# Performance work log

Hardware: AMD Instinct MI355X
Metric: run time of the kernel (lower is better)

Reference implementation:

```python
import jax, jax.numpy as jnp
import numpy as np

N = 100000      # nodes
E = 1600000     # edges (avg degree 16)
IN = 128        # in_channels
H = 128         # hidden
C = 40          # num_classes
NCOMM = 1000    # number of communities


def setup_inputs() -> dict:
    key = jax.random.key(0)
    ks = jax.random.split(key, 6)
    x = jax.random.normal(ks[0], (N, IN), dtype=jnp.float32)
    edge_index = jax.random.randint(ks[1], (2, E), 0, N, dtype=jnp.int64)
    community = jax.random.randint(ks[2], (N,), 0, NCOMM, dtype=jnp.int64)
    W_in = jax.random.normal(ks[3], (2 * IN, H), dtype=jnp.float32) * 0.05
    b_in = jnp.zeros((H,), dtype=jnp.float32)
    W1 = jax.random.normal(ks[4], (H, H), dtype=jnp.float32) * 0.05
    b1 = jnp.zeros((H,), dtype=jnp.float32)
    W2 = jax.random.normal(ks[5], (H, C), dtype=jnp.float32) * 0.05
    b2 = jnp.zeros((C,), dtype=jnp.float32)
    return {"x": x, "edge_index": edge_index, "community": community,
            "W_in": W_in, "b_in": b_in, "W1": W1, "b1": b1, "W2": W2, "b2": b2}


def _gcn_conv(h, W, b, src, dst, n):
    """PyG GCNConv: transform, add self-loops, symmetric deg^-1/2 normalization."""
    hw = h @ W  # [n, out]
    deg = jax.ops.segment_sum(jnp.ones((src.shape[0],), hw.dtype), dst, num_segments=n) + 1.0  # +1 self-loop
    dis = jax.lax.rsqrt(deg)                      # deg >= 1 always
    norm = dis[src] * dis[dst]                    # [E]
    agg = jax.ops.segment_sum(hw[src] * norm[:, None], dst, num_segments=n)
    # self-loop contribution: norm_ii = dis[i]^2 = 1/deg[i]
    return agg + hw * (1.0 / deg)[:, None] + b


def reference(x, edge_index, community, W_in, b_in, W1, b1, W2, b2):
    n = x.shape[0]
    # CommunityPassing(aggr='mean'): per-community mean, broadcast back to nodes
    csum = jax.ops.segment_sum(x, community, num_segments=NCOMM)
    ccnt = jax.ops.segment_sum(jnp.ones((n,), x.dtype), community, num_segments=NCOMM)
    cmean = csum / jnp.maximum(ccnt, 1.0)[:, None]
    x_comm = cmean[community]                     # [n, IN]
    h = jnp.concatenate([x, x_comm], axis=-1)     # [n, 2*IN]
    h = jax.nn.relu(h @ W_in + b_in)              # dropout is identity at eval
    src, dst = edge_index[0], edge_index[1]
    h = jax.nn.relu(_gcn_conv(h, W1, b1, src, dst, n))
    out = _gcn_conv(h, W2, b2, src, dst, n)
    return out
```

## Files before the change

kernel.cpp:

```cpp
#include <hip/hip_runtime.h>
#include <cstdint>
#include <cstddef>

#define NNODES 100000
#define NEDGES 1600000
#define INCH   128
#define HID    128
#define NCLS   40
#define NCOMM_ 1000

#define NBLK  128
#define EPB   (NEDGES/NBLK)
#define NBUCK ((NNODES+255)/256)
#define NCNT  (NBLK*NBUCK)

typedef unsigned int uint32;
typedef unsigned short ushort16;
typedef short s16x8 __attribute__((ext_vector_type(8)));
typedef float f32x4 __attribute__((ext_vector_type(4)));

static __device__ __forceinline__ float4 ld4(const float* p){ return *reinterpret_cast<const float4*>(p); }

static __device__ __forceinline__ unsigned short f2b(float f){
  union{float f; uint32 u;} v; v.f=f;
  uint32 r = v.u + 0x7fffu + ((v.u>>16)&1u);
  return (unsigned short)(r>>16);
}
static __device__ __forceinline__ float b2f(unsigned short h){
  union{uint32 u; float f;} v; v.u = ((uint32)h)<<16; return v.f;
}
static __device__ __forceinline__ float lo16f(uint32 u){ return __int_as_float((int)(u<<16)); }
static __device__ __forceinline__ float hi16f(uint32 u){ return __int_as_float((int)(u&0xffff0000u)); }

static __device__ __forceinline__ void acc8(float* a, uint4 v, float nr){
  a[0]=fmaf(lo16f(v.x),nr,a[0]); a[1]=fmaf(hi16f(v.x),nr,a[1]);
  a[2]=fmaf(lo16f(v.y),nr,a[2]); a[3]=fmaf(hi16f(v.y),nr,a[3]);
  a[4]=fmaf(lo16f(v.z),nr,a[4]); a[5]=fmaf(hi16f(v.z),nr,a[5]);
  a[6]=fmaf(lo16f(v.w),nr,a[6]); a[7]=fmaf(hi16f(v.w),nr,a[7]);
}
static __device__ __forceinline__ void acc4(float* a, uint2 v, float nr){
  a[0]=fmaf(lo16f(v.x),nr,a[0]); a[1]=fmaf(hi16f(v.x),nr,a[1]);
  a[2]=fmaf(lo16f(v.y),nr,a[2]); a[3]=fmaf(hi16f(v.y),nr,a[3]);
}

__global__ void k_ccomm(const int* __restrict__ comm, int* __restrict__ ccnt){
  int i=blockIdx.x*blockDim.x+threadIdx.x;
  if(i<NNODES) atomicAdd(&ccnt[comm[i]],1);
}

__global__ __launch_bounds__(256) void k_bcnt(const int* __restrict__ ei, int* __restrict__ cnt){
  __shared__ int h[NBUCK];
  int t=threadIdx.x, blk=blockIdx.x;
  for(int i=t;i<NBUCK;i+=256) h[i]=0;
  __syncthreads();
  int base=blk*EPB;
  for(int j=t;j<EPB;j+=256){
    int d=ei[NEDGES+base+j];
    atomicAdd(&h[d>>8],1);
  }
  __syncthreads();
  for(int i=t;i<NBUCK;i+=256) cnt[i*NBLK+blk]=h[i];
}

__global__ void k_scan1(const int* __restrict__ in, int n, int* __restrict__ part){
  int t=threadIdx.x, b=blockIdx.x;
  int base=b*1024+t*4, s=0;
  #pragma unroll
  for(int j=0;j<4;j++){ int i=base+j; if(i<n) s+=in[i]; }
  #pragma unroll
  for(int off=32;off>0;off>>=1) s+=__shfl_down(s,off,64);
  __shared__ int wm[4];
  if((t&63)==0) wm[t>>6]=s;
  __syncthreads();
  if(t==0) part[b]=wm[0]+wm[1]+wm[2]+wm[3];
}

__global__ void k_scan2(int* __restrict__ part, int P){
  __shared__ int sm[256];
  int t=threadIdx.x;
  int v=(t<P)?part[t]:0;
  sm[t]=v; __syncthreads();
  #pragma unroll
  for(int off=1;off<256;off<<=1){
    int u=(t>=off)?sm[t-off]:0;
    __syncthreads();
    sm[t]+=u;
    __syncthreads();
  }
  if(t<P) part[t]=(t==0)?0:sm[t-1];
  if(t==0) part[P]=sm[255];
}

__global__ void k_scan3(const int* __restrict__ in, int n, const int* __restrict__ part, int P,
                        int* __restrict__ out){
  int t=threadIdx.x,b=blockIdx.x;
  int base=b*1024+t*4;
  int v[4], ts=0;
  #pragma unroll
  for(int j=0;j<4;j++){ v[j]=(base+j<n)?in[base+j]:0; ts+=v[j]; }
  int lane=t&63, w=t>>6, sc=ts;
  #pragma unroll
  for(int off=1;off<64;off<<=1){ int u=__shfl_up(sc,off,64); if(lane>=off) sc+=u; }
  __shared__ int wm[4];
  if(lane==63) wm[w]=sc;
  __syncthreads();
  int woff=0;
  for(int i=0;i<w;i++) woff+=wm[i];
  int pos=part[b]+woff+sc-ts;
  #pragma unroll
  for(int j=0;j<4;j++){ if(base+j<n) out[base+j]=pos; pos+=v[j]; }
  if(b==0 && t==0) out[n]=part[P];
}

__global__ void k_bextract(const int* __restrict__ cntx, int* __restrict__ brow, int* __restrict__ rp){
  int b=blockIdx.x*blockDim.x+threadIdx.x;
  if(b<NBUCK) brow[b]=cntx[b*NBLK];
  if(b==NBUCK){ brow[NBUCK]=NEDGES; rp[NNODES]=NEDGES; }
}

__global__ __launch_bounds__(256) void k_bscatter(const int* __restrict__ ei, const int* __restrict__ cntx,
                                                  int2* __restrict__ ebuf){
  __shared__ int offs[NBUCK];
  int t=threadIdx.x, blk=blockIdx.x;
  for(int i=t;i<NBUCK;i+=256) offs[i]=cntx[i*NBLK+blk];
  __syncthreads();
  int base=blk*EPB;
  for(int j=t;j<EPB;j+=256){
    int e=base+j;
    int s=ei[e], d=ei[NEDGES+e];
    int p=atomicAdd(&offs[d>>8],1);
    ebuf[p]=make_int2(s,d);
  }
}

__global__ __launch_bounds__(256) void k_bcsr(const int2* __restrict__ ebuf, const int* __restrict__ brow,
                                              int* __restrict__ rp, float* __restrict__ dis,
                                              float* __restrict__ dinv, int* __restrict__ esrc){
  __shared__ int lcnt[256], lrp[256], lfill[256];
  int b=blockIdx.x, t=threadIdx.x;
  int e0=brow[b], e1=brow[b+1];
  int n0=b*256, nloc=min(256, NNODES-n0);
  lcnt[t]=0;
  __syncthreads();
  for(int e=e0+t;e<e1;e+=256){
    int d=ebuf[e].y;
    atomicAdd(&lcnt[d&255],1);
  }
  __syncthreads();
  lrp[t]=lcnt[t]; __syncthreads();
  #pragma unroll
  for(int off=1;off<256;off<<=1){
    int u=(t>=off)?lrp[t-off]:0;
    __syncthreads();
    lrp[t]+=u;
    __syncthreads();
  }
  int excl=lrp[t]-lcnt[t];
  __syncthreads();
  lrp[t]=e0+excl;
  lfill[t]=0;
  if(t<nloc){
    int gid=n0+t;
    rp[gid]=e0+excl;
    float dd=(float)(lcnt[t]+1);
    dis[gid]=rsqrtf(dd);
    dinv[gid]=1.0f/dd;
  }
  __syncthreads();
  for(int e=e0+t;e<e1;e+=256){
    int2 r=ebuf[e];
    int lr=r.y&255;
    int slot=atomicAdd(&lfill[lr],1);
    esrc[lrp[lr]+slot]=r.x;
  }
}

__global__ void k_fill_comm(const int* __restrict__ comm, const int* __restrict__ crow, int* __restrict__ cfill,
                            int* __restrict__ cnode){
  int i=blockIdx.x*blockDim.x+threadIdx.x;
  if(i<NNODES){
    int c=comm[i];
    int p=crow[c]+atomicAdd(&cfill[c],1);
    cnode[p]=i;
  }
}

__global__ void k_comm_mean(const float* __restrict__ x, const int* __restrict__ crow,
                            const int* __restrict__ cnode, float* __restrict__ cmean){
  int c=blockIdx.x; int f=threadIdx.x;
  int a=crow[c], b=crow[c+1];
  float s=0.f;
  for(int j=a;j<b;j++){
    int nd=cnode[j];
    s += x[(size_t)nd*INCH + f];
  }
  float cnt=(float)(b-a);
  cmean[(size_t)c*INCH + f] = s / fmaxf(cnt,1.0f);
}

__global__ void k_wprep(const float* __restrict__ W_in, const float* __restrict__ W1, const float* __restrict__ W2,
                        ushort16* __restrict__ Wt0h, ushort16* __restrict__ Wt0l,
                        ushort16* __restrict__ Wt1h, ushort16* __restrict__ Wt1l,
                        ushort16* __restrict__ Wt2h, ushort16* __restrict__ Wt2l){
  int t = blockIdx.x*256 + threadIdx.x;
  float v; ushort16* ph; ushort16* pl; int off;
  if(t < 32768){
    int n=t>>8, k=t&255; v=W_in[k*128+n]; ph=Wt0h; pl=Wt0l; off=t;
  } else if(t < 49152){
    int u=t-32768; int n=u>>7, k=u&127; v=W1[k*128+n]; ph=Wt1h; pl=Wt1l; off=u;
  } else if(t < 55296){
    int u=t-49152; int n=u>>7, k=u&127; v=(n<40)?W2[k*40+n]:0.f; ph=Wt2h; pl=Wt2l; off=u;
  } else return;
  unsigned short h=f2b(v); unsigned short lo=f2b(v-b2f(h));
  ph[off]=h; pl[off]=lo;
}

template<int K, bool CONCAT, bool BIAS, bool RELU>
__global__ __launch_bounds__(256) void k_mm128(const void* __restrict__ A0, const float* __restrict__ A1f,
                                               const int* __restrict__ comm,
                                               const ushort16* __restrict__ WtH, const ushort16* __restrict__ WtL,
                                               const float* __restrict__ bias,
                                               ushort16* __restrict__ out, int M){
  __shared__ __align__(16) ushort16 As[128*40];
  __shared__ __align__(16) ushort16 Bh[128*40];
  __shared__ __align__(16) ushort16 Bl[128*40];
  int t=threadIdx.x;
  int m0=blockIdx.x*128;
  int lane=t&63, w=t>>6;
  int g=lane>>4, r15=lane&15;

  f32x4 acc0[8], acc1[8];
  #pragma unroll
  for(int i=0;i<8;i++){ acc0[i]=(f32x4){0,0,0,0}; acc1[i]=(f32x4){0,0,0,0}; }

  int ar = t>>1, ko = (t&1)*16;

  for(int kc=0;kc<K;kc+=32){
    __syncthreads();
    {
      s16x8 q0, q1;
      int gr = m0 + ar;
      if(gr < M){
        if(CONCAT){
          const float* src = (kc<128) ? ((const float*)A0 + (size_t)gr*128 + kc + ko)
                                      : (A1f + (size_t)comm[gr]*128 + (kc-128) + ko);
          float4 p0=ld4(src), p1=ld4(src+4), p2=ld4(src+8), p3=ld4(src+12);
          q0[0]=(short)f2b(p0.x); q0[1]=(short)f2b(p0.y); q0[2]=(short)f2b(p0.z); q0[3]=(short)f2b(p0.w);
          q0[4]=(short)f2b(p1.x); q0[5]=(short)f2b(p1.y); q0[6]=(short)f2b(p1.z); q0[7]=(short)f2b(p1.w);
          q1[0]=(short)f2b(p2.x); q1[1]=(short)f2b(p2.y); q1[2]=(short)f2b(p2.z); q1[3]=(short)f2b(p2.w);
          q1[4]=(short)f2b(p3.x); q1[5]=(short)f2b(p3.y); q1[6]=(short)f2b(p3.z); q1[7]=(short)f2b(p3.w);
        } else {
          const ushort16* srcu = (const ushort16*)A0 + (size_t)gr*K + kc + ko;
          q0 = *(const s16x8*)srcu;
          q1 = *(const s16x8*)(srcu+8);
        }
      } else {
        q0=(s16x8){0,0,0,0,0,0,0,0}; q1=q0;
      }
      ushort16* dst=&As[ar*40+ko];
      *(s16x8*)dst=q0; *(s16x8*)(dst+8)=q1;
    }
    {
      const ushort16* sh=&WtH[(size_t)ar*K + kc + ko];
      s16x8 b0=*(const s16x8*)sh, b1=*(const s16x8*)(sh+8);
      ushort16* dh=&Bh[ar*40+ko];
      *(s16x8*)dh=b0; *(s16x8*)(dh+8)=b1;
      const ushort16* sl=&WtL[(size_t)ar*K + kc + ko];
      s16x8 c0=*(const s16x8*)sl, c1=*(const s16x8*)(sl+8);
      ushort16* dl=&Bl[ar*40+ko];
      *(s16x8*)dl=c0; *(s16x8*)(dl+8)=c1;
    }
    __syncthreads();
    s16x8 a0 = *(const s16x8*)&As[(w*32      + r15)*40 + g*8];
    s16x8 a1 = *(const s16x8*)&As[(w*32 + 16 + r15)*40 + g*8];
    #pragma unroll
    for(int tn=0;tn<8;tn++){
      s16x8 bh = *(const s16x8*)&Bh[(tn*16 + r15)*40 + g*8];
      s16x8 bl = *(const s16x8*)&Bl[(tn*16 + r15)*40 + g*8];
      acc0[tn] = __builtin_amdgcn_mfma_f32_16x16x32_bf16(a0, bh, acc0[tn], 0,0,0);
      acc0[tn] = __builtin_amdgcn_mfma_f32_16x16x32_bf16(a0, bl, acc0[tn], 0,0,0);
      acc1[tn] = __builtin_amdgcn_mfma_f32_16x16x32_bf16(a1, bh, acc1[tn], 0,0,0);
      acc1[tn] = __builtin_amdgcn_mfma_f32_16x16x32_bf16(a1, bl, acc1[tn], 0,0,0);
    }
  }

  #pragma unroll
  for(int tn=0;tn<8;tn++){
    int col = tn*16 + r15;
    float bv = BIAS ? bias[col] : 0.f;
    #pragma unroll
    for(int rr=0;rr<4;rr++){
      int row0 = m0 + w*32 + g*4 + rr;
      if(row0 < M){
        float v = acc0[tn][rr] + bv;
        if(RELU) v = fmaxf(v, 0.f);
        out[(size_t)row0*128 + col] = f2b(v);
      }
      int row1 = m0 + w*32 + 16 + g*4 + rr;
      if(row1 < M){
        float v = acc1[tn][rr] + bv;
        if(RELU) v = fmaxf(v, 0.f);
        out[(size_t)row1*128 + col] = f2b(v);
      }
    }
  }
}

__global__ __launch_bounds__(256) void k_mm40(const ushort16* __restrict__ A0,
                                              const ushort16* __restrict__ WtH, const ushort16* __restrict__ WtL,
                                              ushort16* __restrict__ out, int M){
  __shared__ __align__(16) ushort16 As[128*40];
  __shared__ __align__(16) ushort16 Bh[48*40];
  __shared__ __align__(16) ushort16 Bl[48*40];
  int t=threadIdx.x;
  int m0=blockIdx.x*128;
  int lane=t&63, w=t>>6;
  int g=lane>>4, r15=lane&15;

  f32x4 acc0[3], acc1[3];
  #pragma unroll
  for(int i=0;i<3;i++){ acc0[i]=(f32x4){0,0,0,0}; acc1[i]=(f32x4){0,0,0,0}; }

  int ar=t>>1, ko=(t&1)*16;

  for(int kc=0;kc<128;kc+=32){
    __syncthreads();
    {
      s16x8 q0,q1;
      int gr=m0+ar;
      if(gr<M){
        const ushort16* srcu = A0 + (size_t)gr*128 + kc + ko;
        q0=*(const s16x8*)srcu; q1=*(const s16x8*)(srcu+8);
      } else { q0=(s16x8){0,0,0,0,0,0,0,0}; q1=q0; }
      ushort16* dst=&As[ar*40+ko];
      *(s16x8*)dst=q0; *(s16x8*)(dst+8)=q1;
    }
    if(t<96){
      int n=t>>1, k2=(t&1)*16;
      const ushort16* sh=&WtH[(size_t)n*128 + kc + k2];
      s16x8 b0=*(const s16x8*)sh, b1=*(const s16x8*)(sh+8);
      ushort16* dh=&Bh[n*40+k2];
      *(s16x8*)dh=b0; *(s16x8*)(dh+8)=b1;
    } else if(t<192){
      int u=t-96; int n=u>>1, k2=(u&1)*16;
      const ushort16* sl=&WtL[(size_t)n*128 + kc + k2];
      s16x8 c0=*(const s16x8*)sl, c1=*(const s16x8*)(sl+8);
      ushort16* dl=&Bl[n*40+k2];
      *(s16x8*)dl=c0; *(s16x8*)(dl+8)=c1;
    }
    __syncthreads();
    s16x8 a0=*(const s16x8*)&As[(w*32      + r15)*40 + g*8];
    s16x8 a1=*(const s16x8*)&As[(w*32 + 16 + r15)*40 + g*8];
    #pragma unroll
    for(int tn=0;tn<3;tn++){
      s16x8 bh=*(const s16x8*)&Bh[(tn*16 + r15)*40 + g*8];
      s16x8 bl=*(const s16x8*)&Bl[(tn*16 + r15)*40 + g*8];
      acc0[tn]=__builtin_amdgcn_mfma_f32_16x16x32_bf16(a0,bh,acc0[tn],0,0,0);
      acc0[tn]=__builtin_amdgcn_mfma_f32_16x16x32_bf16(a0,bl,acc0[tn],0,0,0);
      acc1[tn]=__builtin_amdgcn_mfma_f32_16x16x32_bf16(a1,bh,acc1[tn],0,0,0);
      acc1[tn]=__builtin_amdgcn_mfma_f32_16x16x32_bf16(a1,bl,acc1[tn],0,0,0);
    }
  }
  #pragma unroll
  for(int tn=0;tn<3;tn++){
    int col=tn*16+r15;
    if(col<NCLS){
      #pragma unroll
      for(int rr=0;rr<4;rr++){
        int row0=m0+w*32+g*4+rr;
        if(row0<M) out[(size_t)row0*NCLS+col]=f2b(acc0[tn][rr]);
        int row1=m0+w*32+16+g*4+rr;
        if(row1<M) out[(size_t)row1*NCLS+col]=f2b(acc1[tn][rr]);
      }
    }
  }
}

__global__ __launch_bounds__(256) void k_agg_h(const uint4* __restrict__ hwv, const int* __restrict__ rp,
                                               const int* __restrict__ esrc,
                                               const float* __restrict__ dis, const float* __restrict__ dinv,
                                               const float* __restrict__ bias, uint4* __restrict__ h1v){
  int w=threadIdx.x>>6;
  int i=blockIdx.x*4+w;
  if(i>=NNODES) return;
  int lane=threadIdx.x&63;
  int g=lane>>4, f=lane&15;
  int e0=rp[i], e1=rp[i+1];
  float di=dis[i];
  float a[8]={0,0,0,0,0,0,0,0};
  int e=e0+g;
  for(; e+4<e1; e+=8){
    int s0=esrc[e], s1=esrc[e+4];
    float n0=di*dis[s0], n1=di*dis[s1];
    uint4 v0=hwv[(size_t)s0*16+f];
    uint4 v1=hwv[(size_t)s1*16+f];
    acc8(a,v0,n0); acc8(a,v1,n1);
  }
  if(e<e1){
    int s0=esrc[e];
    float n0=di*dis[s0];
    uint4 v0=hwv[(size_t)s0*16+f];
    acc8(a,v0,n0);
  }
  #pragma unroll
  for(int k=0;k<8;k++){
    a[k]+=__shfl_xor(a[k],16);
    a[k]+=__shfl_xor(a[k],32);
  }
  if(g==0){
    uint4 sv=hwv[(size_t)i*16+f];
    float dv=dinv[i];
    float4 bA=*reinterpret_cast<const float4*>(&bias[8*f]);
    float4 bB=*reinterpret_cast<const float4*>(&bias[8*f+4]);
    float o0=fmaxf(fmaf(lo16f(sv.x),dv,a[0])+bA.x,0.f);
    float o1=fmaxf(fmaf(hi16f(sv.x),dv,a[1])+bA.y,0.f);
    float o2=fmaxf(fmaf(lo16f(sv.y),dv,a[2])+bA.z,0.f);
    float o3=fmaxf(fmaf(hi16f(sv.y),dv,a[3])+bA.w,0.f);
    float o4=fmaxf(fmaf(lo16f(sv.z),dv,a[4])+bB.x,0.f);
    float o5=fmaxf(fmaf(hi16f(sv.z),dv,a[5])+bB.y,0.f);
    float o6=fmaxf(fmaf(lo16f(sv.w),dv,a[6])+bB.z,0.f);
    float o7=fmaxf(fmaf(hi16f(sv.w),dv,a[7])+bB.w,0.f);
    uint4 o;
    o.x=((uint32)f2b(o1)<<16)|(uint32)f2b(o0);
    o.y=((uint32)f2b(o3)<<16)|(uint32)f2b(o2);
    o.z=((uint32)f2b(o5)<<16)|(uint32)f2b(o4);
    o.w=((uint32)f2b(o7)<<16)|(uint32)f2b(o6);
    h1v[(size_t)i*16+f]=o;
  }
}

__global__ __launch_bounds__(256) void k_agg_out(const uint2* __restrict__ hv, const int* __restrict__ rp,
                                                 const int* __restrict__ esrc,
                                                 const float* __restrict__ dis, const float* __restrict__ dinv,
                                                 const float* __restrict__ bias, float* __restrict__ out){
  int w=threadIdx.x>>6;
  int i=blockIdx.x*4+w;
  if(i>=NNODES) return;
  int lane=threadIdx.x&63;
  int g=lane>>4, f=lane&15;
  bool act=(f<10);
  int e0=rp[i], e1=rp[i+1];
  float di=dis[i];
  float a[4]={0,0,0,0};
  int e=e0+g;
  for(; e+4<e1; e+=8){
    int s0=esrc[e], s1=esrc[e+4];
    float n0=di*dis[s0], n1=di*dis[s1];
    if(act){
      uint2 v0=hv[(size_t)s0*10+f];
      uint2 v1=hv[(size_t)s1*10+f];
      acc4(a,v0,n0); acc4(a,v1,n1);
    }
  }
  if(e<e1){
    int s0=esrc[e];
    float n0=di*dis[s0];
    if(act){
      uint2 v0=hv[(size_t)s0*10+f];
      acc4(a,v0,n0);
    }
  }
  #pragma unroll
  for(int k=0;k<4;k++){
    a[k]+=__shfl_xor(a[k],16);
    a[k]+=__shfl_xor(a[k],32);
  }
  if(g==0 && act){
    uint2 sv=hv[(size_t)i*10+f];
    float dv=dinv[i];
    float4 b=*reinterpret_cast<const float4*>(&bias[4*f]);
    float4 o;
    o.x=fmaf(lo16f(sv.x),dv,a[0])+b.x;
    o.y=fmaf(hi16f(sv.x),dv,a[1])+b.y;
    o.z=fmaf(lo16f(sv.y),dv,a[2])+b.z;
    o.w=fmaf(hi16f(sv.y),dv,a[3])+b.w;
    *reinterpret_cast<float4*>(&out[(size_t)i*40+4*f])=o;
  }
}

extern "C" void kernel_launch(void* const* d_in, const int* in_sizes, int n_in,
                              void* d_out, int out_size, void* d_ws, size_t ws_size,
                              hipStream_t stream) {
  const float* x    = (const float*)d_in[0];
  const int*   ei   = (const int*)  d_in[1];
  const int*   comm = (const int*)  d_in[2];
  const float* W_in = (const float*)d_in[3];
  const float* b_in = (const float*)d_in[4];
  const float* W1   = (const float*)d_in[5];
  const float* b1   = (const float*)d_in[6];
  const float* W2   = (const float*)d_in[7];
  const float* b2   = (const float*)d_in[8];
  float* out = (float*)d_out;

  char* base=(char*)d_ws; size_t off=0;
  auto alloc=[&](size_t bytes)->void*{ void* p=base+off; off=(off+bytes+255)&~(size_t)255; return p; };

  int* zz    =(int*)alloc((size_t)(2*NCOMM_)*4);
  int* ccnt  = zz;
  int* cfill = zz + NCOMM_;
  int* cnt   =(int*)alloc((size_t)NCNT*4);
  int* cntx  =(int*)alloc((size_t)(NCNT+1)*4);
  int* partA =(int*)alloc(64*4);
  int* brow  =(int*)alloc((size_t)(NBUCK+1)*4);
  int* rp    =(int*)alloc((size_t)(NNODES+1)*4);
  int* crow  =(int*)alloc((size_t)(NCOMM_+1)*4);
  int* partB =(int*)alloc(16*4);
  int2* ebuf =(int2*)alloc((size_t)NEDGES*8);
  int* esrc  =(int*)alloc((size_t)NEDGES*4);
  int* cnode =(int*)alloc((size_t)NNODES*4);
  float* dis =(float*)alloc((size_t)NNODES*4);
  float* dinv=(float*)alloc((size_t)NNODES*4);
  float* cmean=(float*)alloc((size_t)NCOMM_*INCH*4);
  ushort16* h0 =(ushort16*)alloc((size_t)NNODES*HID*2);
  ushort16* hw =(ushort16*)alloc((size_t)NNODES*HID*2);
  ushort16* Wt0h=(ushort16*)alloc(32768*2);
  ushort16* Wt0l=(ushort16*)alloc(32768*2);
  ushort16* Wt1h=(ushort16*)alloc(16384*2);
  ushort16* Wt1l=(ushort16*)alloc(16384*2);
  ushort16* Wt2h=(ushort16*)alloc(6144*2);
  ushort16* Wt2l=(ushort16*)alloc(6144*2);

  hipMemsetAsync(zz, 0, (size_t)(2*NCOMM_)*4, stream);

  int gN=(NNODES+255)/256;

  k_bcnt    <<<NBLK,256,0,stream>>>(ei, cnt);
  int PC=(NCNT+1023)/1024;
  k_scan1<<<PC,256,0,stream>>>(cnt, NCNT, partA);
  k_scan2<<<1,256,0,stream>>>(partA, PC);
  k_scan3<<<PC,256,0,stream>>>(cnt, NCNT, partA, PC, cntx);
  k_bextract<<<(NBUCK+256)/256,256,0,stream>>>(cntx, brow, rp);
  k_bscatter<<<NBLK,256,0,stream>>>(ei, cntx, ebuf);
  k_bcsr    <<<NBUCK,256,0,stream>>>(ebuf, brow, rp, dis, dinv, esrc);

  k_ccomm<<<gN,256,0,stream>>>(comm, ccnt);
  int PB=(NCOMM_+1023)/1024;
  k_scan1<<<PB,256,0,stream>>>(ccnt, NCOMM_, partB);
  k_scan2<<<1,256,0,stream>>>(partB, PB);
  k_scan3<<<PB,256,0,stream>>>(ccnt, NCOMM_, partB, PB, crow);
  k_fill_comm<<<gN,256,0,stream>>>(comm, crow, cfill, cnode);
  k_comm_mean<<<NCOMM_,128,0,stream>>>(x, crow, cnode, cmean);
  k_wprep<<<216,256,0,stream>>>(W_in, W1, W2, Wt0h, Wt0l, Wt1h, Wt1l, Wt2h, Wt2l);

  int gM=(NNODES+127)/128;
  k_mm128<256,true,true,true><<<gM,256,0,stream>>>(x, cmean, comm, Wt0h, Wt0l, b_in, h0, NNODES);
  k_mm128<128,false,false,false><<<gM,256,0,stream>>>(h0, nullptr, nullptr, Wt1h, Wt1l, nullptr, hw, NNODES);
  int gA=(NNODES+3)/4;
  k_agg_h<<<gA,256,0,stream>>>((const uint4*)hw, rp, esrc, dis, dinv, b1, (uint4*)h0);
  k_mm40<<<gM,256,0,stream>>>(h0, Wt2h, Wt2l, hw, NNODES);
  k_agg_out<<<gA,256,0,stream>>>((const uint2*)hw, rp, esrc, dis, dinv, b2, out);
}
```

Before: 472.7 us.

## Pack edge buffer, pre-convert x to bf16, unroll aggregation with packed FMAs

Shrinks the bucketed edge buffer from int2 to one packed uint32 (17-bit source plus 8-bit local destination), halving scatter and CSR-build traffic. Adds a kernel that converts x to bf16 up front and stores community means as bf16, so the first GEMM loads bf16 directly instead of converting fp32 in its inner loop; the community index is also hoisted out of the k-loop. The aggregation kernels unroll to four edges per iteration and use 2-wide float vector FMAs to raise memory-level parallelism. The extra conversion pass adds a full read and write of x in exchange for lighter GEMM loads.

```diff
diff --git a/kernel.cpp b/kernel.cpp
--- a/kernel.cpp
+++ b/kernel.cpp
@@ -18,6 +18,7 @@
 typedef unsigned short ushort16;
 typedef short s16x8 __attribute__((ext_vector_type(8)));
 typedef float f32x4 __attribute__((ext_vector_type(4)));
+typedef float f32x2 __attribute__((ext_vector_type(2)));
 
 static __device__ __forceinline__ float4 ld4(const float* p){ return *reinterpret_cast<const float4*>(p); }
 
@@ -32,20 +33,37 @@
 static __device__ __forceinline__ float lo16f(uint32 u){ return __int_as_float((int)(u<<16)); }
 static __device__ __forceinline__ float hi16f(uint32 u){ return __int_as_float((int)(u&0xffff0000u)); }
 
-static __device__ __forceinline__ void acc8(float* a, uint4 v, float nr){
-  a[0]=fmaf(lo16f(v.x),nr,a[0]); a[1]=fmaf(hi16f(v.x),nr,a[1]);
-  a[2]=fmaf(lo16f(v.y),nr,a[2]); a[3]=fmaf(hi16f(v.y),nr,a[3]);
-  a[4]=fmaf(lo16f(v.z),nr,a[4]); a[5]=fmaf(hi16f(v.z),nr,a[5]);
-  a[6]=fmaf(lo16f(v.w),nr,a[6]); a[7]=fmaf(hi16f(v.w),nr,a[7]);
-}
-static __device__ __forceinline__ void acc4(float* a, uint2 v, float nr){
-  a[0]=fmaf(lo16f(v.x),nr,a[0]); a[1]=fmaf(hi16f(v.x),nr,a[1]);
-  a[2]=fmaf(lo16f(v.y),nr,a[2]); a[3]=fmaf(hi16f(v.y),nr,a[3]);
+static __device__ __forceinline__ f32x2 up2(uint32 u){
+  union{uint2 u2; f32x2 f;} c;
+  c.u2.x = u<<16; c.u2.y = u&0xffff0000u;
+  return c.f;
+}
+static __device__ __forceinline__ void acc8p(f32x2* a, uint4 v, float nr){
+  f32x2 n; n[0]=nr; n[1]=nr;
+  a[0] += up2(v.x)*n;
+  a[1] += up2(v.y)*n;
+  a[2] += up2(v.z)*n;
+  a[3] += up2(v.w)*n;
+}
+static __device__ __forceinline__ void acc4p(f32x2* a, uint2 v, float nr){
+  f32x2 n; n[0]=nr; n[1]=nr;
+  a[0] += up2(v.x)*n;
+  a[1] += up2(v.y)*n;
 }
 
 __global__ void k_ccomm(const int* __restrict__ comm, int* __restrict__ ccnt){
   int i=blockIdx.x*blockDim.x+threadIdx.x;
   if(i<NNODES) atomicAdd(&ccnt[comm[i]],1);
+}
+
+__global__ __launch_bounds__(256) void k_xprep(const float* __restrict__ x, ushort16* __restrict__ xb){
+  size_t i=(size_t)(blockIdx.x*256u+threadIdx.x)*8u;
+  if(i>=(size_t)NNODES*INCH) return;
+  float4 p0=ld4(x+i), p1=ld4(x+i+4);
+  s16x8 q;
+  q[0]=(short)f2b(p0.x); q[1]=(short)f2b(p0.y); q[2]=(short)f2b(p0.z); q[3]=(short)f2b(p0.w);
+  q[4]=(short)f2b(p1.x); q[5]=(short)f2b(p1.y); q[6]=(short)f2b(p1.z); q[7]=(short)f2b(p1.w);
+  *(s16x8*)(xb+i)=q;
 }
 
 __global__ __launch_bounds__(256) void k_bcnt(const int* __restrict__ ei, int* __restrict__ cnt){
@@ -119,7 +137,7 @@
 }
 
 __global__ __launch_bounds__(256) void k_bscatter(const int* __restrict__ ei, const int* __restrict__ cntx,
-                                                  int2* __restrict__ ebuf){
+                                                  uint32* __restrict__ ebuf){
   __shared__ int offs[NBUCK];
   int t=threadIdx.x, blk=blockIdx.x;
   for(int i=t;i<NBUCK;i+=256) offs[i]=cntx[i*NBLK+blk];
@@ -129,11 +147,11 @@
     int e=base+j;
     int s=ei[e], d=ei[NEDGES+e];
     int p=atomicAdd(&offs[d>>8],1);
-    ebuf[p]=make_int2(s,d);
-  }
-}
-
-__global__ __launch_bounds__(256) void k_bcsr(const int2* __restrict__ ebuf, const int* __restrict__ brow,
+    ebuf[p]=(uint32)s | (((uint32)d&255u)<<17);
+  }
+}
+
+__global__ __launch_bounds__(256) void k_bcsr(const uint32* __restrict__ ebuf, const int* __restrict__ brow,
                                               int* __restrict__ rp, float* __restrict__ dis,
                                               float* __restrict__ dinv, int* __restrict__ esrc){
   __shared__ int lcnt[256], lrp[256], lfill[256];
@@ -143,8 +161,7 @@
   lcnt[t]=0;
   __syncthreads();
   for(int e=e0+t;e<e1;e+=256){
-    int d=ebuf[e].y;
-    atomicAdd(&lcnt[d&255],1);
+    atomicAdd(&lcnt[ebuf[e]>>17],1);
   }
   __syncthreads();
   lrp[t]=lcnt[t]; __syncthreads();
@@ -168,10 +185,10 @@
   }
   __syncthreads();
   for(int e=e0+t;e<e1;e+=256){
-    int2 r=ebuf[e];
-    int lr=r.y&255;
+    uint32 r=ebuf[e];
+    int lr=r>>17;
     int slot=atomicAdd(&lfill[lr],1);
-    esrc[lrp[lr]+slot]=r.x;
+    esrc[lrp[lr]+slot]=(int)(r&0x1ffffu);
   }
 }
 
@@ -186,7 +203,7 @@
 }
 
 __global__ void k_comm_mean(const float* __restrict__ x, const int* __restrict__ crow,
-                            const int* __restrict__ cnode, float* __restrict__ cmean){
+                            const int* __restrict__ cnode, ushort16* __restrict__ cmb){
   int c=blockIdx.x; int f=threadIdx.x;
   int a=crow[c], b=crow[c+1];
   float s=0.f;
@@ -195,7 +212,7 @@
     s += x[(size_t)nd*INCH + f];
   }
   float cnt=(float)(b-a);
-  cmean[(size_t)c*INCH + f] = s / fmaxf(cnt,1.0f);
+  cmb[(size_t)c*INCH + f] = f2b(s / fmaxf(cnt,1.0f));
 }
 
 __global__ void k_wprep(const float* __restrict__ W_in, const float* __restrict__ W1, const float* __restrict__ W2,
@@ -216,7 +233,7 @@
 }
 
 template<int K, bool CONCAT, bool BIAS, bool RELU>
-__global__ __launch_bounds__(256) void k_mm128(const void* __restrict__ A0, const float* __restrict__ A1f,
+__global__ __launch_bounds__(256) void k_mm128(const ushort16* __restrict__ A0, const ushort16* __restrict__ A1,
                                                const int* __restrict__ comm,
                                                const ushort16* __restrict__ WtH, const ushort16* __restrict__ WtL,
                                                const float* __restrict__ bias,
@@ -234,26 +251,23 @@
   for(int i=0;i<8;i++){ acc0[i]=(f32x4){0,0,0,0}; acc1[i]=(f32x4){0,0,0,0}; }
 
   int ar = t>>1, ko = (t&1)*16;
+  int gr = m0 + ar;
+  int cm = (CONCAT && gr<M) ? comm[gr] : 0;
 
   for(int kc=0;kc<K;kc+=32){
     __syncthreads();
     {
       s16x8 q0, q1;
-      int gr = m0 + ar;
       if(gr < M){
+        const ushort16* srcu;
         if(CONCAT){
-          const float* src = (kc<128) ? ((const float*)A0 + (size_t)gr*128 + kc + ko)
-                                      : (A1f + (size_t)comm[gr]*128 + (kc-128) + ko);
-          float4 p0=ld4(src), p1=ld4(src+4), p2=ld4(src+8), p3=ld4(src+12);
-          q0[0]=(short)f2b(p0.x); q0[1]=(short)f2b(p0.y); q0[2]=(short)f2b(p0.z); q0[3]=(short)f2b(p0.w);
-          q0[4]=(short)f2b(p1.x); q0[5]=(short)f2b(p1.y); q0[6]=(short)f2b(p1.z); q0[7]=(short)f2b(p1.w);
-          q1[0]=(short)f2b(p2.x); q1[1]=(short)f2b(p2.y); q1[2]=(short)f2b(p2.z); q1[3]=(short)f2b(p2.w);
-          q1[4]=(short)f2b(p3.x); q1[5]=(short)f2b(p3.y); q1[6]=(short)f2b(p3.z); q1[7]=(short)f2b(p3.w);
+          srcu = (kc<128) ? (A0 + (size_t)gr*128 + kc + ko)
+                          : (A1 + (size_t)cm*128 + (kc-128) + ko);
         } else {
-          const ushort16* srcu = (const ushort16*)A0 + (size_t)gr*K + kc + ko;
-          q0 = *(const s16x8*)srcu;
-          q1 = *(const s16x8*)(srcu+8);
+          srcu = A0 + (size_t)gr*K + kc + ko;
         }
+        q0 = *(const s16x8*)srcu;
+        q1 = *(const s16x8*)(srcu+8);
       } else {
         q0=(s16x8){0,0,0,0,0,0,0,0}; q1=q0;
       }
@@ -387,39 +401,43 @@
   int g=lane>>4, f=lane&15;
   int e0=rp[i], e1=rp[i+1];
   float di=dis[i];
-  float a[8]={0,0,0,0,0,0,0,0};
+  f32x2 a[4];
+  a[0]=(f32x2){0,0}; a[1]=(f32x2){0,0}; a[2]=(f32x2){0,0}; a[3]=(f32x2){0,0};
   int e=e0+g;
-  for(; e+4<e1; e+=8){
-    int s0=esrc[e], s1=esrc[e+4];
-    float n0=di*dis[s0], n1=di*dis[s1];
+  for(; e+12<e1; e+=16){
+    int s0=esrc[e], s1=esrc[e+4], s2=esrc[e+8], s3=esrc[e+12];
+    float n0=di*dis[s0], n1=di*dis[s1], n2=di*dis[s2], n3=di*dis[s3];
     uint4 v0=hwv[(size_t)s0*16+f];
     uint4 v1=hwv[(size_t)s1*16+f];
-    acc8(a,v0,n0); acc8(a,v1,n1);
-  }
-  if(e<e1){
+    uint4 v2=hwv[(size_t)s2*16+f];
+    uint4 v3=hwv[(size_t)s3*16+f];
+    acc8p(a,v0,n0); acc8p(a,v1,n1); acc8p(a,v2,n2); acc8p(a,v3,n3);
+  }
+  for(; e<e1; e+=4){
     int s0=esrc[e];
     float n0=di*dis[s0];
     uint4 v0=hwv[(size_t)s0*16+f];
-    acc8(a,v0,n0);
-  }
+    acc8p(a,v0,n0);
+  }
+  float* af=(float*)a;
   #pragma unroll
   for(int k=0;k<8;k++){
-    a[k]+=__shfl_xor(a[k],16);
-    a[k]+=__shfl_xor(a[k],32);
+    af[k]+=__shfl_xor(af[k],16);
+    af[k]+=__shfl_xor(af[k],32);
   }
   if(g==0){
     uint4 sv=hwv[(size_t)i*16+f];
     float dv=dinv[i];
     float4 bA=*reinterpret_cast<const float4*>(&bias[8*f]);
     float4 bB=*reinterpret_cast<const float4*>(&bias[8*f+4]);
-    float o0=fmaxf(fmaf(lo16f(sv.x),dv,a[0])+bA.x,0.f);
-    float o1=fmaxf(fmaf(hi16f(sv.x),dv,a[1])+bA.y,0.f);
-    float o2=fmaxf(fmaf(lo16f(sv.y),dv,a[2])+bA.z,0.f);
-    float o3=fmaxf(fmaf(hi16f(sv.y),dv,a[3])+bA.w,0.f);
-    float o4=fmaxf(fmaf(lo16f(sv.z),dv,a[4])+bB.x,0.f);
-    float o5=fmaxf(fmaf(hi16f(sv.z),dv,a[5])+bB.y,0.f);
-    float o6=fmaxf(fmaf(lo16f(sv.w),dv,a[6])+bB.z,0.f);
-    float o7=fmaxf(fmaf(hi16f(sv.w),dv,a[7])+bB.w,0.f);
+    float o0=fmaxf(fmaf(lo16f(sv.x),dv,af[0])+bA.x,0.f);
+    float o1=fmaxf(fmaf(hi16f(sv.x),dv,af[1])+bA.y,0.f);
+    float o2=fmaxf(fmaf(lo16f(sv.y),dv,af[2])+bA.z,0.f);
+    float o3=fmaxf(fmaf(hi16f(sv.y),dv,af[3])+bA.w,0.f);
+    float o4=fmaxf(fmaf(lo16f(sv.z),dv,af[4])+bB.x,0.f);
+    float o5=fmaxf(fmaf(hi16f(sv.z),dv,af[5])+bB.y,0.f);
+    float o6=fmaxf(fmaf(lo16f(sv.w),dv,af[6])+bB.z,0.f);
+    float o7=fmaxf(fmaf(hi16f(sv.w),dv,af[7])+bB.w,0.f);
     uint4 o;
     o.x=((uint32)f2b(o1)<<16)|(uint32)f2b(o0);
     o.y=((uint32)f2b(o3)<<16)|(uint32)f2b(o2);
@@ -441,39 +459,43 @@
   bool act=(f<10);
   int e0=rp[i], e1=rp[i+1];
   float di=dis[i];
-  float a[4]={0,0,0,0};
+  f32x2 a[2];
+  a[0]=(f32x2){0,0}; a[1]=(f32x2){0,0};
   int e=e0+g;
-  for(; e+4<e1; e+=8){
-    int s0=esrc[e], s1=esrc[e+4];
-    float n0=di*dis[s0], n1=di*dis[s1];
+  for(; e+12<e1; e+=16){
+    int s0=esrc[e], s1=esrc[e+4], s2=esrc[e+8], s3=esrc[e+12];
+    float n0=di*dis[s0], n1=di*dis[s1], n2=di*dis[s2], n3=di*dis[s3];
     if(act){
       uint2 v0=hv[(size_t)s0*10+f];
       uint2 v1=hv[(size_t)s1*10+f];
-      acc4(a,v0,n0); acc4(a,v1,n1);
-    }
-  }
-  if(e<e1){
+      uint2 v2=hv[(size_t)s2*10+f];
+      uint2 v3=hv[(size_t)s3*10+f];
+      acc4p(a,v0,n0); acc4p(a,v1,n1); acc4p(a,v2,n2); acc4p(a,v3,n3);
+    }
+  }
+  for(; e<e1; e+=4){
     int s0=esrc[e];
     float n0=di*dis[s0];
     if(act){
       uint2 v0=hv[(size_t)s0*10+f];
-      acc4(a,v0,n0);
-    }
-  }
+      acc4p(a,v0,n0);
+    }
+  }
+  float* af=(float*)a;
   #pragma unroll
   for(int k=0;k<4;k++){
-    a[k]+=__shfl_xor(a[k],16);
-    a[k]+=__shfl_xor(a[k],32);
+    af[k]+=__shfl_xor(af[k],16);
+    af[k]+=__shfl_xor(af[k],32);
   }
   if(g==0 && act){
     uint2 sv=hv[(size_t)i*10+f];
     float dv=dinv[i];
     float4 b=*reinterpret_cast<const float4*>(&bias[4*f]);
     float4 o;
-    o.x=fmaf(lo16f(sv.x),dv,a[0])+b.x;
-    o.y=fmaf(hi16f(sv.x),dv,a[1])+b.y;
-    o.z=fmaf(lo16f(sv.y),dv,a[2])+b.z;
-    o.w=fmaf(hi16f(sv.y),dv,a[3])+b.w;
+    o.x=fmaf(lo16f(sv.x),dv,af[0])+b.x;
+    o.y=fmaf(hi16f(sv.x),dv,af[1])+b.y;
+    o.z=fmaf(lo16f(sv.y),dv,af[2])+b.z;
+    o.w=fmaf(hi16f(sv.y),dv,af[3])+b.w;
     *reinterpret_cast<float4*>(&out[(size_t)i*40+4*f])=o;
   }
 }
@@ -505,12 +527,13 @@
   int* rp    =(int*)alloc((size_t)(NNODES+1)*4);
   int* crow  =(int*)alloc((size_t)(NCOMM_+1)*4);
   int* partB =(int*)alloc(16*4);
-  int2* ebuf =(int2*)alloc((size_t)NEDGES*8);
+  uint32* ebuf=(uint32*)alloc((size_t)NEDGES*4);
   int* esrc  =(int*)alloc((size_t)NEDGES*4);
   int* cnode =(int*)alloc((size_t)NNODES*4);
   float* dis =(float*)alloc((size_t)NNODES*4);
   float* dinv=(float*)alloc((size_t)NNODES*4);
-  float* cmean=(float*)alloc((size_t)NCOMM_*INCH*4);
+  ushort16* xb  =(ushort16*)alloc((size_t)NNODES*INCH*2);
+  ushort16* cmb =(ushort16*)alloc((size_t)NCOMM_*INCH*2);
   ushort16* h0 =(ushort16*)alloc((size_t)NNODES*HID*2);
   ushort16* hw =(ushort16*)alloc((size_t)NNODES*HID*2);
   ushort16* Wt0h=(ushort16*)alloc(32768*2);
@@ -533,17 +556,19 @@
   k_bscatter<<<NBLK,256,0,stream>>>(ei, cntx, ebuf);
   k_bcsr    <<<NBUCK,256,0,stream>>>(ebuf, brow, rp, dis, dinv, esrc);
 
+  k_xprep<<<6250,256,0,stream>>>(x, xb);
+
   k_ccomm<<<gN,256,0,stream>>>(comm, ccnt);
   int PB=(NCOMM_+1023)/1024;
   k_scan1<<<PB,256,0,stream>>>(ccnt, NCOMM_, partB);
   k_scan2<<<1,256,0,stream>>>(partB, PB);
   k_scan3<<<PB,256,0,stream>>>(ccnt, NCOMM_, partB, PB, crow);
   k_fill_comm<<<gN,256,0,stream>>>(comm, crow, cfill, cnode);
-  k_comm_mean<<<NCOMM_,128,0,stream>>>(x, crow, cnode, cmean);
+  k_comm_mean<<<NCOMM_,128,0,stream>>>(x, crow, cnode, cmb);
   k_wprep<<<216,256,0,stream>>>(W_in, W1, W2, Wt0h, Wt0l, Wt1h, Wt1l, Wt2h, Wt2l);
 
   int gM=(NNODES+127)/128;
-  k_mm128<256,true,true,true><<<gM,256,0,stream>>>(x, cmean, comm, Wt0h, Wt0l, b_in, h0, NNODES);
+  k_mm128<256,true,true,true><<<gM,256,0,stream>>>(xb, cmb, comm, Wt0h, Wt0l, b_in, h0, NNODES);
   k_mm128<128,false,false,false><<<gM,256,0,stream>>>(h0, nullptr, nullptr, Wt1h, Wt1l, nullptr, hw, NNODES);
   int gA=(NNODES+3)/4;
   k_agg_h<<<gA,256,0,stream>>>((const uint4*)hw, rp, esrc, dis, dinv, b1, (uint4*)h0);
```

After: 464.3 us. Within noise of the previous version (-1.8%).
